# Optimization experiments

Hardware: AMD Instinct MI355X
Metric: run time of the kernel (lower is better)

The kernel has to match this reference:

```python
import jax, jax.numpy as jnp
import numpy as np

NUM_HEADS = 16
EPS = 1e-15


def setup_inputs() -> dict:
    key = jax.random.key(0)
    k1, k2, k3, k4 = jax.random.split(key, 4)
    B, N, C = 4, 16384, 512
    x = jax.random.normal(k1, (B, N, C), dtype=jnp.float32)
    qkv_weight = jax.random.normal(k2, (3 * C, C), dtype=jnp.float32) * 0.02
    proj_weight = jax.random.normal(k3, (C, C), dtype=jnp.float32) * 0.02
    proj_bias = jax.random.normal(k4, (C,), dtype=jnp.float32) * 0.02
    return {"x": x, "qkv_weight": qkv_weight, "proj_weight": proj_weight, "proj_bias": proj_bias}


def reference(x, qkv_weight, proj_weight, proj_bias):
    B, N, C = x.shape
    H = NUM_HEADS
    D = C // H
    # fused linear + ReLU on q,k (v stays linear, per backward: grad_v has no relu mask)
    qkv = (x @ qkv_weight.T).reshape(B, N, 3, C)
    q = jax.nn.relu(qkv[:, :, 0]).reshape(B, N, H, D)
    k = jax.nn.relu(qkv[:, :, 1]).reshape(B, N, H, D)
    v = qkv[:, :, 2].reshape(B, N, H, D)
    qf = q.astype(jnp.float32)
    kf = k.astype(jnp.float32)
    vf = v.astype(jnp.float32)
    # pad v with a ones column -> normalizer row in vk (pad_vk_mm_fwd)
    v_pad = jnp.concatenate([vf, jnp.ones_like(vf[..., :1])], axis=-1)  # [B,N,H,D+1]
    vk = jnp.einsum('bnhc,bnhd->bhcd', v_pad, kf)  # [B,H,D+1,D] accumulated in fp32
    vk_q = jnp.einsum('bnhd,bhcd->bnhc', qf, vk)  # [B,N,H,D+1]
    # fused division by normalizer (vk_q_mm_divide_fwd)
    proj_input = (vk_q[..., :-1] / (vk_q[..., -1:] + EPS)).astype(x.dtype).reshape(B, N, C)
    return proj_input @ proj_weight.T + proj_bias
```

## Files before the change

### kernel.cpp

```cpp
#include <hip/hip_runtime.h>
#include <stdint.h>

#define NB 4
#define SEQ 16384
#define CH 512
#define NH 16
#define HD 32
#define QKVC 1536
#define MROWS (NB * SEQ)

typedef unsigned short u16;
typedef __attribute__((ext_vector_type(8))) short bf16x8;
typedef __attribute__((ext_vector_type(4))) float f32x4;

__device__ __forceinline__ float bf2f(u16 u) {
  union { unsigned int i; float f; } c; c.i = ((unsigned int)u) << 16; return c.f;
}
__device__ __forceinline__ u16 f2bf(float f) {
  union { float f; unsigned int i; } c; c.f = f;
  return (u16)((c.i + 0x7fffu + ((c.i >> 16) & 1u)) >> 16);
}

__device__ __forceinline__ void async16(const u16* g, u16* l) {
  __builtin_amdgcn_global_load_lds((const __attribute__((address_space(1))) void*)g,
                                   (__attribute__((address_space(3))) void*)l,
                                   16, 0, 0);
}

__global__ void prep_kernel(const float* __restrict__ x,
                            const float* __restrict__ qw,
                            const float* __restrict__ pw,
                            u16* __restrict__ xb,
                            u16* __restrict__ qwb,
                            u16* __restrict__ pwb,
                            float* __restrict__ vk) {
  int gid = blockIdx.x * blockDim.x + threadIdx.x;
  int stride = gridDim.x * blockDim.x;

  const float4* x4 = (const float4*)x;
  ushort4* xb4 = (ushort4*)xb;
  for (int i = gid; i < (MROWS * CH / 4); i += stride) {
    float4 v = x4[i];
    ushort4 o; o.x = f2bf(v.x); o.y = f2bf(v.y); o.z = f2bf(v.z); o.w = f2bf(v.w);
    xb4[i] = o;
  }
  const float4* q4 = (const float4*)qw;
  ushort4* qwb4 = (ushort4*)qwb;
  for (int i = gid; i < (QKVC * CH / 4); i += stride) {
    float4 v = q4[i];
    ushort4 o; o.x = f2bf(v.x); o.y = f2bf(v.y); o.z = f2bf(v.z); o.w = f2bf(v.w);
    qwb4[i] = o;
  }
  const float4* p4 = (const float4*)pw;
  ushort4* pwb4 = (ushort4*)pwb;
  for (int i = gid; i < (CH * CH / 4); i += stride) {
    float4 v = p4[i];
    ushort4 o; o.x = f2bf(v.x); o.y = f2bf(v.y); o.z = f2bf(v.z); o.w = f2bf(v.w);
    pwb4[i] = o;
  }
  float4 z; z.x = 0.f; z.y = 0.f; z.z = 0.f; z.w = 0.f;
  float4* vk4 = (float4*)vk;
  for (int i = gid; i < (NB * NH * 33 * 32 / 4); i += stride) vk4[i] = z;
}

template <int N_DIM, bool SPLIT3, bool FINAL>
__global__ __launch_bounds__(512, 2) void gemm8p_kernel(
    const u16* __restrict__ A, const u16* __restrict__ Bm,
    void* __restrict__ Out, u16* __restrict__ OutK, u16* __restrict__ OutV,
    const float* __restrict__ bias) {
  __shared__ __align__(16) u16 lds[65536];

  const int tid = threadIdx.x;
  const int lane = tid & 63;
  const int w = tid >> 6;
  const int wr = w >> 2;
  const int wc = w & 3;
  const int fr = lane & 15;
  const int g = lane >> 4;
  const int xr = (fr & 7) << 3;

  const int gridX = N_DIM / 256;
  const int nwg = gridX * (MROWS / 256);
  int bid = blockIdx.y * gridX + blockIdx.x;
  bid = (bid & 7) * (nwg >> 3) + (bid >> 3);
  const long row0 = (long)(bid / gridX) * 256;
  const long col0 = (long)(bid % gridX) * 256;

  const int trow = tid >> 3;
  const int tcol = ((tid & 7) * 8) ^ (((tid >> 3) & 7) << 3);

#define STAGE_A(kt_, h_)                                                      \
  do {                                                                        \
    u16* lb_ = &lds[(((kt_) & 1) * 2 + (h_)) * 8192 + w * 512];               \
    const u16* ga_ = A + (size_t)(row0 + (h_) * 128 + trow) * 512 +           \
                     (kt_) * 64 + tcol;                                       \
    async16(ga_, lb_);                                                        \
    async16(ga_ + 64 * 512, lb_ + 4096);                                      \
  } while (0)

#define STAGE_B(kt_, h_)                                                      \
  do {                                                                        \
    u16* lb_ = &lds[32768 + (((kt_) & 1) * 2 + (h_)) * 8192 + w * 512];       \
    const u16* gb_ = Bm + (size_t)(col0 + (h_) * 128 + trow) * 512 +          \
                     (kt_) * 64 + tcol;                                       \
    async16(gb_, lb_);                                                        \
    async16(gb_ + 64 * 512, lb_ + 4096);                                      \
  } while (0)

  f32x4 acc[8][4];
#pragma unroll
  for (int m = 0; m < 8; m++)
#pragma unroll
    for (int n = 0; n < 4; n++) {
      f32x4 z = {0.f, 0.f, 0.f, 0.f};
      acc[m][n] = z;
    }
  bf16x8 a[4][2], b[4][2];

  STAGE_B(0, 0); STAGE_A(0, 0); STAGE_B(0, 1); STAGE_A(0, 1);
  STAGE_B(1, 0); STAGE_A(1, 0);
  asm volatile("s_waitcnt vmcnt(4)" ::: "memory");
  __builtin_amdgcn_s_barrier();

#pragma unroll
  for (int kt = 0; kt < 8; ++kt) {
    const int abase = ((kt & 1) * 2 + wr) * 8192;
    const int bbase = 32768 + ((kt & 1) * 2 + (wc >> 1)) * 8192 + (wc & 1) * 4096;

#pragma unroll
    for (int m = 0; m < 4; ++m)
#pragma unroll
      for (int kk = 0; kk < 2; ++kk)
        a[m][kk] = *(const bf16x8*)&lds[abase + (m * 16 + fr) * 64 + ((kk * 32 + g * 8) ^ xr)];
#pragma unroll
    for (int n = 0; n < 2; ++n)
#pragma unroll
      for (int kk = 0; kk < 2; ++kk)
        b[n][kk] = *(const bf16x8*)&lds[bbase + (n * 16 + fr) * 64 + ((kk * 32 + g * 8) ^ xr)];
    if (kt < 7) STAGE_B(kt + 1, 1);
    __builtin_amdgcn_s_barrier();
    asm volatile("s_waitcnt lgkmcnt(0)" ::: "memory");
    __builtin_amdgcn_s_setprio(1);
#pragma unroll
    for (int m = 0; m < 4; ++m)
#pragma unroll
      for (int n = 0; n < 2; ++n)
#pragma unroll
        for (int kk = 0; kk < 2; ++kk)
          acc[m][n] = __builtin_amdgcn_mfma_f32_16x16x32_bf16(a[m][kk], b[n][kk], acc[m][n], 0, 0, 0);
    __builtin_amdgcn_s_setprio(0);
    __builtin_amdgcn_s_barrier();

#pragma unroll
    for (int n = 0; n < 2; ++n)
#pragma unroll
      for (int kk = 0; kk < 2; ++kk)
        b[2 + n][kk] = *(const bf16x8*)&lds[bbase + ((n + 2) * 16 + fr) * 64 + ((kk * 32 + g * 8) ^ xr)];
    if (kt < 7) STAGE_A(kt + 1, 1);
    __builtin_amdgcn_s_barrier();
    asm volatile("s_waitcnt lgkmcnt(0)" ::: "memory");
    __builtin_amdgcn_s_setprio(1);
#pragma unroll
    for (int m = 0; m < 4; ++m)
#pragma unroll
      for (int n = 0; n < 2; ++n)
#pragma unroll
        for (int kk = 0; kk < 2; ++kk)
          acc[m][2 + n] = __builtin_amdgcn_mfma_f32_16x16x32_bf16(a[m][kk], b[2 + n][kk], acc[m][2 + n], 0, 0, 0);
    __builtin_amdgcn_s_setprio(0);
    __builtin_amdgcn_s_barrier();

#pragma unroll
    for (int m = 0; m < 4; ++m)
#pragma unroll
      for (int kk = 0; kk < 2; ++kk)
        a[m][kk] = *(const bf16x8*)&lds[abase + ((m + 4) * 16 + fr) * 64 + ((kk * 32 + g * 8) ^ xr)];
    if (kt < 6) STAGE_B(kt + 2, 0);
    __builtin_amdgcn_s_barrier();
    asm volatile("s_waitcnt lgkmcnt(0)" ::: "memory");
    __builtin_amdgcn_s_setprio(1);
#pragma unroll
    for (int m = 0; m < 4; ++m)
#pragma unroll
      for (int n = 0; n < 2; ++n)
#pragma unroll
        for (int kk = 0; kk < 2; ++kk)
          acc[4 + m][2 + n] = __builtin_amdgcn_mfma_f32_16x16x32_bf16(a[m][kk], b[2 + n][kk], acc[4 + m][2 + n], 0, 0, 0);
    __builtin_amdgcn_s_setprio(0);
    __builtin_amdgcn_s_barrier();

    if (kt < 6) {
      STAGE_A(kt + 2, 0);
      asm volatile("s_waitcnt vmcnt(4)" ::: "memory");
    } else {
      asm volatile("s_waitcnt vmcnt(0)" ::: "memory");
    }
    __builtin_amdgcn_s_barrier();
    __builtin_amdgcn_s_setprio(1);
#pragma unroll
    for (int m = 0; m < 4; ++m)
#pragma unroll
      for (int n = 0; n < 2; ++n)
#pragma unroll
        for (int kk = 0; kk < 2; ++kk)
          acc[4 + m][n] = __builtin_amdgcn_mfma_f32_16x16x32_bf16(a[m][kk], b[n][kk], acc[4 + m][n], 0, 0, 0);
    __builtin_amdgcn_s_setprio(0);
    __builtin_amdgcn_s_barrier();
  }
#undef STAGE_A
#undef STAGE_B

  const long rbase = row0 + wr * 128;
  if constexpr (SPLIT3) {
    const int bufi = (int)(col0 >> 9);
    u16* ob = bufi == 0 ? (u16*)Out : (bufi == 1 ? OutK : OutV);
    const bool dorelu = bufi < 2;
    const long cbase = (col0 & 511) + wc * 64;
#pragma unroll
    for (int m = 0; m < 8; ++m)
#pragma unroll
      for (int n = 0; n < 4; ++n)
#pragma unroll
        for (int j = 0; j < 4; ++j) {
          long gr = rbase + m * 16 + g * 4 + j;
          long gc = cbase + n * 16 + fr;
          float v = acc[m][n][j];
          if (dorelu) v = fmaxf(v, 0.f);
          ob[gr * 512 + gc] = f2bf(v);
        }
  } else {
    const long cbase = col0 + wc * 64;
#pragma unroll
    for (int m = 0; m < 8; ++m)
#pragma unroll
      for (int n = 0; n < 4; ++n)
#pragma unroll
        for (int j = 0; j < 4; ++j) {
          long gr = rbase + m * 16 + g * 4 + j;
          long gc = cbase + n * 16 + fr;
          float v = acc[m][n][j];
          if constexpr (FINAL) {
            ((float*)Out)[gr * N_DIM + gc] = v + bias[gc];
          } else {
            ((u16*)Out)[gr * N_DIM + gc] = f2bf(v);
          }
        }
  }
}

__global__ __launch_bounds__(256) void vk_kernel(const u16* __restrict__ kb,
                                                 const u16* __restrict__ vb,
                                                 float* __restrict__ vk) {
  __shared__ u16 tile[4][64 * 64];
  __shared__ float red[1056];

  const int tid = threadIdx.x;
  const int lane = tid & 63;
  const int w = tid >> 6;

  for (int i = tid; i < 1056; i += 256) red[i] = 0.f;
  __syncthreads();

  const int bh = blockIdx.x >> 4;
  const int split = blockIdx.x & 15;
  const int b = bh >> 4, h = bh & 15;

  const int s = lane & 7;
  const int rl = lane >> 3;
  const u16* src = (s & 4) ? vb : kb;
  const size_t gbase = (size_t)b * SEQ * 512 + h * 32 + (s & 3) * 8;

  f32x4 acc[2][2];
  f32x4 accs[2];
#pragma unroll
  for (int tc = 0; tc < 2; tc++) {
    f32x4 z = {0.f, 0.f, 0.f, 0.f};
    accs[tc] = z;
#pragma unroll
    for (int td = 0; td < 2; td++) acc[tc][td] = z;
  }
  bf16x8 ones;
#pragma unroll
  for (int j = 0; j < 8; j++) ones[j] = (short)0x3F80;

  const int m = lane & 15;
  const int g = lane >> 4;
  u16* tw = tile[w];
  const int n0w = split * 1024 + w * 256;

  for (int t = 0; t < 4; ++t) {
    const int nt = n0w + t * 64;
#pragma unroll
    for (int p = 0; p < 8; ++p)
      async16(src + gbase + (size_t)(nt + p * 8 + rl) * 512, &tw[p * 512]);
    asm volatile("s_waitcnt vmcnt(0)" ::: "memory");
#pragma unroll
    for (int kk = 0; kk < 2; ++kk) {
      bf16x8 av[2], bk[2];
#pragma unroll
      for (int tc = 0; tc < 2; tc++)
#pragma unroll
        for (int j = 0; j < 8; j++)
          av[tc][j] = (short)tw[(kk * 32 + g * 8 + j) * 64 + 32 + tc * 16 + m];
#pragma unroll
      for (int td = 0; td < 2; td++)
#pragma unroll
        for (int j = 0; j < 8; j++)
          bk[td][j] = (short)tw[(kk * 32 + g * 8 + j) * 64 + td * 16 + m];
#pragma unroll
      for (int tc = 0; tc < 2; tc++)
#pragma unroll
        for (int td = 0; td < 2; td++)
          acc[tc][td] = __builtin_amdgcn_mfma_f32_16x16x32_bf16(av[tc], bk[td], acc[tc][td], 0, 0, 0);
#pragma unroll
      for (int td = 0; td < 2; td++)
        accs[td] = __builtin_amdgcn_mfma_f32_16x16x32_bf16(ones, bk[td], accs[td], 0, 0, 0);
    }
  }

#pragma unroll
  for (int tc = 0; tc < 2; tc++)
#pragma unroll
    for (int td = 0; td < 2; td++)
#pragma unroll
      for (int j = 0; j < 4; j++)
        atomicAdd(&red[(tc * 16 + g * 4 + j) * 32 + td * 16 + m], acc[tc][td][j]);
  if (lane < 16) {
#pragma unroll
    for (int td = 0; td < 2; td++)
      atomicAdd(&red[1024 + td * 16 + lane], accs[td][0]);
  }
  __syncthreads();
  float* dst = vk + (size_t)bh * 1056;
  for (int i = tid; i < 1056; i += 256) atomicAdd(&dst[i], red[i]);
}

__global__ __launch_bounds__(256) void vkq_kernel(const u16* __restrict__ qb,
                                                  const float* __restrict__ vk,
                                                  u16* __restrict__ pi) {
  __shared__ float vkl[8 * 1056];
  __shared__ u16 ob[32 * 256];

  const int tid = threadIdx.x;
  const int chunk = blockIdx.x & 511;
  const int hh = (blockIdx.x >> 9) & 1;
  const int b = blockIdx.x >> 10;
  const int n0 = chunk * 32;

  const float* vg = vk + (size_t)(b * NH + hh * 8) * 1056;
  for (int i = tid; i < 8 * 1056; i += 256) vkl[i] = vg[i];
  __syncthreads();

  const int nl = tid & 31;
  const int hl = tid >> 5;
  const float* vkh = &vkl[hl * 1056];

  const u16* qp = qb + ((size_t)b * SEQ + n0 + nl) * 512 + (hh * 8 + hl) * 32;
  float qf[32];
#pragma unroll
  for (int s2 = 0; s2 < 4; ++s2) {
    bf16x8 qv = *(const bf16x8*)(qp + s2 * 8);
#pragma unroll
    for (int j = 0; j < 8; ++j) qf[s2 * 8 + j] = bf2f((u16)qv[j]);
  }

  float num[32];
#pragma unroll
  for (int c = 0; c < 32; ++c) {
    float a = 0.f;
#pragma unroll
    for (int d4 = 0; d4 < 8; ++d4) {
      f32x4 vv = *(const f32x4*)&vkh[c * 32 + d4 * 4];
      a = fmaf(qf[d4 * 4 + 0], vv[0], a);
      a = fmaf(qf[d4 * 4 + 1], vv[1], a);
      a = fmaf(qf[d4 * 4 + 2], vv[2], a);
      a = fmaf(qf[d4 * 4 + 3], vv[3], a);
    }
    num[c] = a;
  }
  float den = 0.f;
#pragma unroll
  for (int d4 = 0; d4 < 8; ++d4) {
    f32x4 vv = *(const f32x4*)&vkh[32 * 32 + d4 * 4];
    den = fmaf(qf[d4 * 4 + 0], vv[0], den);
    den = fmaf(qf[d4 * 4 + 1], vv[1], den);
    den = fmaf(qf[d4 * 4 + 2], vv[2], den);
    den = fmaf(qf[d4 * 4 + 3], vv[3], den);
  }
  const float r = 1.0f / (den + 1e-15f);
#pragma unroll
  for (int c = 0; c < 32; ++c) ob[nl * 256 + hl * 32 + c] = f2bf(num[c] * r);
  __syncthreads();

  u16* pg = pi + ((size_t)b * SEQ + n0) * CH + hh * 256;
  for (int i = tid; i < 1024; i += 256) {
    const int n = i >> 5;
    const int u = i & 31;
    *(bf16x8*)(pg + (size_t)n * CH + u * 8) = *(const bf16x8*)&ob[i * 8];
  }
}

extern "C" void kernel_launch(void* const* d_in, const int* in_sizes, int n_in,
                              void* d_out, int out_size, void* d_ws, size_t ws_size,
                              hipStream_t stream) {
  const float* x = (const float*)d_in[0];
  const float* qw = (const float*)d_in[1];
  const float* pw = (const float*)d_in[2];
  const float* bias = (const float*)d_in[3];

  char* ws = (char*)d_ws;
  u16* qb = (u16*)(ws);
  u16* kb = (u16*)(ws + 67108864);
  u16* vb = (u16*)(ws + 134217728);
  u16* xb = (u16*)(ws + 201326592);
  u16* qwb = (u16*)(ws + 268435456);
  u16* pwb = (u16*)(ws + 270008320);
  float* vk = (float*)(ws + 270532608);
  u16* pi = xb;

  prep_kernel<<<2048, 256, 0, stream>>>(x, qw, pw, xb, qwb, pwb, vk);
  gemm8p_kernel<QKVC, true, false>
      <<<dim3(QKVC / 256, MROWS / 256), 512, 0, stream>>>(xb, qwb, qb, kb, vb, nullptr);
  vk_kernel<<<NB * NH * 16, 256, 0, stream>>>(kb, vb, vk);
  vkq_kernel<<<NB * 2 * (SEQ / 32), 256, 0, stream>>>(qb, vk, pi);
  gemm8p_kernel<CH, false, true>
      <<<dim3(CH / 256, MROWS / 256), 512, 0, stream>>>(pi, pwb, d_out, nullptr, nullptr, bias);
}
```

Baseline: 319.6 us.

## Fuse fp32-to-bf16 conversion of x into the QKV GEMM A-tile loader

Removes the separate pass that converts x to bf16. The QKV GEMM now reads fp32 x directly into registers, converts it to bf16 and writes it into swizzled LDS, with register-level prefetch two k-tiles ahead. This saves one full write and read of the bf16 copy of x (64 MB read, 64 MB written). The cost is that each of the six column-block workgroups per row block re-reads fp32 A, which is twice the bytes of bf16 A. It also adds register pressure and synchronous LDS stores in the GEMM's main loop.

```diff
diff --git a/kernel.cpp b/kernel.cpp
--- a/kernel.cpp
+++ b/kernel.cpp
@@ -27,23 +27,14 @@
                                    16, 0, 0);
 }
 
-__global__ void prep_kernel(const float* __restrict__ x,
-                            const float* __restrict__ qw,
+__global__ void prep_kernel(const float* __restrict__ qw,
                             const float* __restrict__ pw,
-                            u16* __restrict__ xb,
                             u16* __restrict__ qwb,
                             u16* __restrict__ pwb,
                             float* __restrict__ vk) {
   int gid = blockIdx.x * blockDim.x + threadIdx.x;
   int stride = gridDim.x * blockDim.x;
 
-  const float4* x4 = (const float4*)x;
-  ushort4* xb4 = (ushort4*)xb;
-  for (int i = gid; i < (MROWS * CH / 4); i += stride) {
-    float4 v = x4[i];
-    ushort4 o; o.x = f2bf(v.x); o.y = f2bf(v.y); o.z = f2bf(v.z); o.w = f2bf(v.w);
-    xb4[i] = o;
-  }
   const float4* q4 = (const float4*)qw;
   ushort4* qwb4 = (ushort4*)qwb;
   for (int i = gid; i < (QKVC * CH / 4); i += stride) {
@@ -63,12 +54,15 @@
   for (int i = gid; i < (NB * NH * 33 * 32 / 4); i += stride) vk4[i] = z;
 }
 
-template <int N_DIM, bool SPLIT3, bool FINAL>
+template <int N_DIM, bool F32A, bool FINAL>
 __global__ __launch_bounds__(512, 2) void gemm8p_kernel(
-    const u16* __restrict__ A, const u16* __restrict__ Bm,
+    const void* __restrict__ Ain, const u16* __restrict__ Bm,
     void* __restrict__ Out, u16* __restrict__ OutK, u16* __restrict__ OutV,
     const float* __restrict__ bias) {
   __shared__ __align__(16) u16 lds[65536];
+
+  const float* A32 = (const float*)Ain;
+  const u16* A16 = (const u16*)Ain;
 
   const int tid = threadIdx.x;
   const int lane = tid & 63;
@@ -87,12 +81,14 @@
   const long col0 = (long)(bid % gridX) * 256;
 
   const int trow = tid >> 3;
-  const int tcol = ((tid & 7) * 8) ^ (((tid >> 3) & 7) << 3);
-
-#define STAGE_A(kt_, h_)                                                      \
+  const int c8lin = (tid & 7) * 8;
+  const int tcol = c8lin ^ ((trow & 7) << 3);
+  const int aswz = c8lin ^ ((trow & 7) << 3);
+
+#define STAGE_A16(kt_, h_)                                                    \
   do {                                                                        \
     u16* lb_ = &lds[(((kt_) & 1) * 2 + (h_)) * 8192 + w * 512];               \
-    const u16* ga_ = A + (size_t)(row0 + (h_) * 128 + trow) * 512 +           \
+    const u16* ga_ = A16 + (size_t)(row0 + (h_) * 128 + trow) * 512 +         \
                      (kt_) * 64 + tcol;                                       \
     async16(ga_, lb_);                                                        \
     async16(ga_ + 64 * 512, lb_ + 4096);                                      \
@@ -107,6 +103,31 @@
     async16(gb_ + 64 * 512, lb_ + 4096);                                      \
   } while (0)
 
+#define LOADA(kt_, s_)                                                        \
+  do {                                                                        \
+    _Pragma("unroll") for (int r4 = 0; r4 < 4; ++r4) {                        \
+      const float* ga_ = A32 + (size_t)(row0 + r4 * 64 + trow) * 512 +        \
+                         (kt_) * 64 + c8lin;                                  \
+      aset[s_][r4][0] = *(const f32x4*)ga_;                                   \
+      aset[s_][r4][1] = *(const f32x4*)(ga_ + 4);                             \
+    }                                                                         \
+  } while (0)
+
+#define WRITEA(kt_, s_)                                                       \
+  do {                                                                        \
+    _Pragma("unroll") for (int r4 = 0; r4 < 4; ++r4) {                        \
+      bf16x8 wv_;                                                             \
+      _Pragma("unroll") for (int j = 0; j < 4; ++j) {                         \
+        wv_[j] = (short)f2bf(aset[s_][r4][0][j]);                             \
+        wv_[4 + j] = (short)f2bf(aset[s_][r4][1][j]);                         \
+      }                                                                       \
+      const int h_ = r4 >> 1;                                                 \
+      const int r_ = (r4 & 1) * 64 + trow;                                    \
+      *(bf16x8*)&lds[(((kt_) & 1) * 2 + h_) * 8192 + r_ * 64 + aswz] = wv_;   \
+    }                                                                         \
+  } while (0)
+
+  f32x4 aset[2][4][2];
   f32x4 acc[8][4];
 #pragma unroll
   for (int m = 0; m < 8; m++)
@@ -117,9 +138,18 @@
     }
   bf16x8 a[4][2], b[4][2];
 
-  STAGE_B(0, 0); STAGE_A(0, 0); STAGE_B(0, 1); STAGE_A(0, 1);
-  STAGE_B(1, 0); STAGE_A(1, 0);
-  asm volatile("s_waitcnt vmcnt(4)" ::: "memory");
+  if constexpr (F32A) {
+    LOADA(0, 0);
+    asm volatile("s_waitcnt vmcnt(0)" ::: "memory");
+    WRITEA(0, 0);
+    LOADA(1, 1);
+    STAGE_B(0, 0); STAGE_B(0, 1); STAGE_B(1, 0);
+    asm volatile("s_waitcnt vmcnt(2) lgkmcnt(0)" ::: "memory");
+  } else {
+    STAGE_B(0, 0); STAGE_A16(0, 0); STAGE_B(0, 1); STAGE_A16(0, 1);
+    STAGE_B(1, 0); STAGE_A16(1, 0);
+    asm volatile("s_waitcnt vmcnt(4)" ::: "memory");
+  }
   __builtin_amdgcn_s_barrier();
 
 #pragma unroll
@@ -137,6 +167,9 @@
 #pragma unroll
       for (int kk = 0; kk < 2; ++kk)
         b[n][kk] = *(const bf16x8*)&lds[bbase + (n * 16 + fr) * 64 + ((kk * 32 + g * 8) ^ xr)];
+    if constexpr (F32A) {
+      if (kt < 6) LOADA(kt + 2, kt & 1);
+    }
     if (kt < 7) STAGE_B(kt + 1, 1);
     __builtin_amdgcn_s_barrier();
     asm volatile("s_waitcnt lgkmcnt(0)" ::: "memory");
@@ -156,7 +189,11 @@
 #pragma unroll
       for (int kk = 0; kk < 2; ++kk)
         b[2 + n][kk] = *(const bf16x8*)&lds[bbase + ((n + 2) * 16 + fr) * 64 + ((kk * 32 + g * 8) ^ xr)];
-    if (kt < 7) STAGE_A(kt + 1, 1);
+    if constexpr (F32A) {
+      if (kt < 7) WRITEA(kt + 1, (kt + 1) & 1);
+    } else {
+      if (kt < 7) STAGE_A16(kt + 1, 1);
+    }
     __builtin_amdgcn_s_barrier();
     asm volatile("s_waitcnt lgkmcnt(0)" ::: "memory");
     __builtin_amdgcn_s_setprio(1);
@@ -189,11 +226,19 @@
     __builtin_amdgcn_s_setprio(0);
     __builtin_amdgcn_s_barrier();
 
-    if (kt < 6) {
-      STAGE_A(kt + 2, 0);
-      asm volatile("s_waitcnt vmcnt(4)" ::: "memory");
+    if constexpr (F32A) {
+      if (kt < 6) {
+        asm volatile("s_waitcnt vmcnt(2)" ::: "memory");
+      } else {
+        asm volatile("s_waitcnt vmcnt(0)" ::: "memory");
+      }
     } else {
-      asm volatile("s_waitcnt vmcnt(0)" ::: "memory");
+      if (kt < 6) {
+        STAGE_A16(kt + 2, 0);
+        asm volatile("s_waitcnt vmcnt(4)" ::: "memory");
+      } else {
+        asm volatile("s_waitcnt vmcnt(0)" ::: "memory");
+      }
     }
     __builtin_amdgcn_s_barrier();
     __builtin_amdgcn_s_setprio(1);
@@ -207,11 +252,13 @@
     __builtin_amdgcn_s_setprio(0);
     __builtin_amdgcn_s_barrier();
   }
-#undef STAGE_A
+#undef STAGE_A16
 #undef STAGE_B
+#undef LOADA
+#undef WRITEA
 
   const long rbase = row0 + wr * 128;
-  if constexpr (SPLIT3) {
+  if constexpr (!FINAL) {
     const int bufi = (int)(col0 >> 9);
     u16* ob = bufi == 0 ? (u16*)Out : (bufi == 1 ? OutK : OutV);
     const bool dorelu = bufi < 2;
@@ -238,12 +285,7 @@
         for (int j = 0; j < 4; ++j) {
           long gr = rbase + m * 16 + g * 4 + j;
           long gc = cbase + n * 16 + fr;
-          float v = acc[m][n][j];
-          if constexpr (FINAL) {
-            ((float*)Out)[gr * N_DIM + gc] = v + bias[gc];
-          } else {
-            ((u16*)Out)[gr * N_DIM + gc] = f2bf(v);
-          }
+          ((float*)Out)[gr * N_DIM + gc] = acc[m][n][j] + bias[gc];
         }
   }
 }
@@ -412,15 +454,14 @@
   u16* qb = (u16*)(ws);
   u16* kb = (u16*)(ws + 67108864);
   u16* vb = (u16*)(ws + 134217728);
-  u16* xb = (u16*)(ws + 201326592);
+  u16* pi = (u16*)(ws + 201326592);
   u16* qwb = (u16*)(ws + 268435456);
   u16* pwb = (u16*)(ws + 270008320);
   float* vk = (float*)(ws + 270532608);
-  u16* pi = xb;
-
-  prep_kernel<<<2048, 256, 0, stream>>>(x, qw, pw, xb, qwb, pwb, vk);
+
+  prep_kernel<<<256, 256, 0, stream>>>(qw, pw, qwb, pwb, vk);
   gemm8p_kernel<QKVC, true, false>
-      <<<dim3(QKVC / 256, MROWS / 256), 512, 0, stream>>>(xb, qwb, qb, kb, vb, nullptr);
+      <<<dim3(QKVC / 256, MROWS / 256), 512, 0, stream>>>(x, qwb, qb, kb, vb, nullptr);
   vk_kernel<<<NB * NH * 16, 256, 0, stream>>>(kb, vb, vk);
   vkq_kernel<<<NB * 2 * (SEQ / 32), 256, 0, stream>>>(qb, vk, pi);
   gemm8p_kernel<CH, false, true>
```

Result: slower. 513.8 us (+60.8%).
